# Kernel tuning notes

Measured on AMD Instinct MI355X. Metric: run time of the kernel, lower is better.

## Reference

```python
import jax, jax.numpy as jnp
import numpy as np

N_Q = 4  # QuantumSampler is hard-wired to 4 qubits (16-dim statevector)


def _build_tables():
    """Static permutation for the CNOT chain and Z-sign table, computed once in numpy."""
    n = N_Q
    dim = 1 << n
    cnots = [(i, (i + 1) % n) for i in range(n)]  # (0,1),(1,2),(2,3),(3,0)
    fmap = np.empty(dim, dtype=np.int64)
    for i in range(dim):
        bits = [(i >> (n - 1 - w)) & 1 for w in range(n)]  # wire w <-> bit (n-1-w)
        for c, t in cnots:
            if bits[c]:
                bits[t] ^= 1
        fmap[i] = sum(b << (n - 1 - w) for w, b in enumerate(bits))
    finv = np.argsort(fmap)  # new_state[j] = old_state[finv[j]]
    signs = np.array([[1.0 - 2.0 * ((j >> (n - 1 - w)) & 1) for w in range(n)]
                      for j in range(dim)], dtype=np.float32)  # <Z_w> signs per basis state
    return jnp.asarray(finv), jnp.asarray(signs)

PERM, SIGNS = _build_tables()


def quantum_gate_probs(q, theta):
    """Simulate: RX(q_w) then RX(theta_w) per wire (angles add), CNOT chain, <Z> per wire, softmax.
    q: [B,4] encoder angles; theta: [4] trainable angles. Returns [B,4] gate probabilities."""
    half = 0.5 * (q + theta)                      # RX(a)RX(b) = RX(a+b)
    c = jnp.cos(half).astype(jnp.complex64)       # amplitude on |0>
    s = (jnp.sin(half).astype(jnp.complex64)) * (-1j)  # amplitude on |1> is -i sin(a/2)
    a = jnp.stack([c, s], axis=-1)                # [B,4,2] single-qubit states
    a0, a1, a2, a3 = a[:, 0], a[:, 1], a[:, 2], a[:, 3]
    # product state |psi> = a0 (x) a1 (x) a2 (x) a3  -> [B,2,2,2,2] -> [B,16]
    st = (a0[:, :, None, None, None] * a1[:, None, :, None, None]
          * a2[:, None, None, :, None] * a3[:, None, None, None, :])
    st = st.reshape(q.shape[0], 16)[:, PERM]      # apply CNOT chain (amplitude permutation)
    probs = st.real ** 2 + st.imag ** 2           # [B,16]
    exps = probs @ SIGNS                          # [B,4] Pauli-Z expectations per wire
    return jax.nn.softmax(exps, axis=-1)


def setup_inputs() -> dict:
    key = jax.random.key(0)
    ks = jax.random.split(key, 8)
    T, B, D, H = 256, 128, 1024, 1024
    inputs = jax.random.normal(ks[0], (T, B, D), dtype=jnp.float32)
    sc_d = 1.0 / np.sqrt(D)
    sc_h = 1.0 / np.sqrt(H)
    return {
        "inputs": inputs,
        "Wi": jax.random.normal(ks[1], (H, D), dtype=jnp.float32) * sc_d,
        "bi": jnp.zeros((H,), dtype=jnp.float32),
        "Wh": jax.random.normal(ks[2], (H, H), dtype=jnp.float32) * sc_h,
        "bh": jnp.zeros((H,), dtype=jnp.float32),
        "Wq": jax.random.normal(ks[3], (4, H), dtype=jnp.float32) * sc_h,
        "bq": jnp.zeros((4,), dtype=jnp.float32),
        "theta": jax.random.uniform(ks[4], (4,), dtype=jnp.float32, minval=-np.pi, maxval=np.pi),
    }


def reference(inputs, Wi, bi, Wh, bh, Wq, bq, theta):
    T, B, _ = inputs.shape
    H = Wi.shape[0]
    hx0 = jnp.zeros((B, H), dtype=inputs.dtype)
    cx0 = jnp.zeros((B, H), dtype=inputs.dtype)

    def step(carry, x):
        hx, cx = carry
        combined = x @ Wi.T + bi + hx @ Wh.T + bh   # [B,H]
        qin = combined @ Wq.T + bq                  # [B,4]
        gates = quantum_gate_probs(qin, theta)      # [B,4]
        f, i_, g, o = gates[:, 0:1], gates[:, 1:2], gates[:, 2:3], gates[:, 3:4]
        cx = f * cx + i_ * jnp.tanh(g)              # broadcast [B,1]*[B,H]
        hx = o * jnp.tanh(cx)
        return (hx, cx), hx

    (hx, cx), ys = jax.lax.scan(step, (hx0, cx0), inputs)
    return ys, hx, cx
```

## Files before the change

### kernel.cpp

```cpp
#include <hip/hip_runtime.h>

#define T_STEPS 256
#define BATCH   128
#define DIM     1024
#define NROWS   (T_STEPS * BATCH)

typedef float vfloat4 __attribute__((ext_vector_type(4)));

#define WS_M     0
#define WS_VP    4096

__global__ __launch_bounds__(256) void k_prep(const float* __restrict__ Wi,
                                              const float* __restrict__ Wh,
                                              const float* __restrict__ bi,
                                              const float* __restrict__ bh,
                                              const float* __restrict__ Wq,
                                              float* __restrict__ M,
                                              float* __restrict__ vpart) {
    int blk  = blockIdx.x;
    int tid  = threadIdx.x;
    int wave = tid >> 6;
    int lane = tid & 63;

    if (blk < 16) {
        int d = blk * 64 + lane;
        const float* wq = Wq + wave * DIM;
        float acc = 0.f;
        for (int j = 0; j < DIM; j += 8) {
            #pragma unroll
            for (int u = 0; u < 8; u++)
                acc += wq[j + u] * Wi[(size_t)(j + u) * DIM + d];
        }
        M[wave * DIM + d] = acc;
    } else {
        int bb = blk - 16;
        __shared__ float red[4][8];
        int j0 = bb * 16 + wave * 4;
        float sv0 = 0.f, sv1 = 0.f, sv2 = 0.f, sv3 = 0.f;
        float sc0 = 0.f, sc1 = 0.f, sc2 = 0.f, sc3 = 0.f;
        #pragma unroll
        for (int jj = 0; jj < 4; jj++) {
            int j = j0 + jj;
            const float4* row = (const float4*)(Wh + (size_t)j * DIM);
            float s = 0.f;
            #pragma unroll
            for (int k = 0; k < 4; k++) {
                float4 t4 = row[k * 64 + lane];
                s += t4.x + t4.y + t4.z + t4.w;
            }
            #pragma unroll
            for (int off = 32; off; off >>= 1) s += __shfl_xor(s, off, 64);
            float bbias = bi[j] + bh[j];
            float q0 = Wq[0 * DIM + j], q1 = Wq[1 * DIM + j];
            float q2 = Wq[2 * DIM + j], q3 = Wq[3 * DIM + j];
            sv0 += q0 * s;  sc0 += q0 * bbias;
            sv1 += q1 * s;  sc1 += q1 * bbias;
            sv2 += q2 * s;  sc2 += q2 * bbias;
            sv3 += q3 * s;  sc3 += q3 * bbias;
        }
        if (lane == 0) {
            red[wave][0] = sv0; red[wave][1] = sv1; red[wave][2] = sv2; red[wave][3] = sv3;
            red[wave][4] = sc0; red[wave][5] = sc1; red[wave][6] = sc2; red[wave][7] = sc3;
        }
        __syncthreads();
        if (tid < 8)
            vpart[bb * 8 + tid] = red[0][tid] + red[1][tid] + red[2][tid] + red[3][tid];
    }
}

__device__ __forceinline__ float fast_tanh(float x) {
    float e = __expf(2.f * x);
    return (e - 1.f) * __builtin_amdgcn_rcpf(e + 1.f);
}

__device__ __forceinline__ void rec_step(float4 qv,
                                         float b0, float b1, float b2, float b3,
                                         float v0, float v1, float v2, float v3,
                                         float& h, float& c) {
    float z0 = __cosf(qv.x + b0 + h * v0);
    float z1 = __cosf(qv.y + b1 + h * v1);
    float z2 = __cosf(qv.z + b2 + h * v2);
    float z3 = __cosf(qv.w + b3 + h * v3);
    float e1 = z0 * z1;
    float e2 = e1 * z2;
    float e3 = e2 * z3;
    float e0 = z1 * z2 * z3;
    float x0 = __expf(e0), x1 = __expf(e1), x2 = __expf(e2), x3 = __expf(e3);
    float inv = __builtin_amdgcn_rcpf(x0 + x1 + x2 + x3);
    float f  = x0 * inv;
    float i_ = x1 * inv;
    float g  = x2 * inv;
    float o  = x3 * inv;
    c = f * c + i_ * fast_tanh(g);
    h = o * fast_tanh(c);
}

__global__ __launch_bounds__(512) void k_main(const float* __restrict__ x,
                                              const float* __restrict__ bq,
                                              const float* __restrict__ theta,
                                              const float* __restrict__ ws,
                                              float* __restrict__ out)
{
    __shared__ float4 qrow[T_STEPS];
    const float*  M   = ws + WS_M;
    const float4* vp4 = (const float4*)(ws + WS_VP);

    const int b    = blockIdx.x;
    const int tid  = threadIdx.x;
    const int wave = tid >> 6;
    const int lane = tid & 63;

    {
        float4 m[4][4];
        #pragma unroll
        for (int w = 0; w < 4; w++)
            #pragma unroll
            for (int k = 0; k < 4; k++)
                m[w][k] = *(const float4*)(M + w * DIM + k * 256 + lane * 4);

        for (int t = wave; t < T_STEPS; t += 8) {
            const float4* row = (const float4*)(x + ((size_t)t * BATCH + b) * DIM);
            float a0 = 0.f, a1 = 0.f, a2 = 0.f, a3 = 0.f;
            #pragma unroll
            for (int k = 0; k < 4; k++) {
                float4 xv = row[k * 64 + lane];
                a0 += xv.x * m[0][k].x + xv.y * m[0][k].y + xv.z * m[0][k].z + xv.w * m[0][k].w;
                a1 += xv.x * m[1][k].x + xv.y * m[1][k].y + xv.z * m[1][k].z + xv.w * m[1][k].w;
                a2 += xv.x * m[2][k].x + xv.y * m[2][k].y + xv.z * m[2][k].z + xv.w * m[2][k].w;
                a3 += xv.x * m[3][k].x + xv.y * m[3][k].y + xv.z * m[3][k].z + xv.w * m[3][k].w;
            }
            #pragma unroll
            for (int off = 32; off; off >>= 1) {
                a0 += __shfl_xor(a0, off, 64);
                a1 += __shfl_xor(a1, off, 64);
                a2 += __shfl_xor(a2, off, 64);
                a3 += __shfl_xor(a3, off, 64);
            }
            if (lane == 0) qrow[t] = make_float4(a0, a1, a2, a3);
        }
    }
    __syncthreads();
    if (wave >= 4) return;

    float4 sa = vp4[lane * 2];
    float4 sc = vp4[lane * 2 + 1];
    #pragma unroll
    for (int off = 32; off; off >>= 1) {
        sa.x += __shfl_xor(sa.x, off, 64);  sa.y += __shfl_xor(sa.y, off, 64);
        sa.z += __shfl_xor(sa.z, off, 64);  sa.w += __shfl_xor(sa.w, off, 64);
        sc.x += __shfl_xor(sc.x, off, 64);  sc.y += __shfl_xor(sc.y, off, 64);
        sc.z += __shfl_xor(sc.z, off, 64);  sc.w += __shfl_xor(sc.w, off, 64);
    }
    const float v0 = sa.x, v1 = sa.y, v2 = sa.z, v3 = sa.w;
    const float b0 = sc.x + bq[0] + theta[0];
    const float b1 = sc.y + bq[1] + theta[1];
    const float b2 = sc.z + bq[2] + theta[2];
    const float b3 = sc.w + bq[3] + theta[3];

    float h = 0.f, c = 0.f;

    #define EMIT_H(tt)                                                           \
        do {                                                                     \
            vfloat4 vv = {h, h, h, h};                                           \
            __builtin_nontemporal_store(vv,                                      \
                (vfloat4*)(out + ((size_t)(tt) * BATCH + b) * DIM + wave * 256)  \
                    + lane);                                                     \
        } while (0)

    float4 q0 = qrow[0], q1 = qrow[1], q2 = qrow[2], q3 = qrow[3];
    float4 q4 = qrow[4], q5 = qrow[5], q6 = qrow[6], q7 = qrow[7];

    for (int t = 0; t < T_STEPS; t += 8) {
        float4 n0, n1, n2, n3, n4, n5, n6, n7;
        if (t + 8 < T_STEPS) {
            n0 = qrow[t + 8];  n1 = qrow[t + 9];
            n2 = qrow[t + 10]; n3 = qrow[t + 11];
            n4 = qrow[t + 12]; n5 = qrow[t + 13];
            n6 = qrow[t + 14]; n7 = qrow[t + 15];
        }
        rec_step(q0, b0, b1, b2, b3, v0, v1, v2, v3, h, c); EMIT_H(t + 0);
        rec_step(q1, b0, b1, b2, b3, v0, v1, v2, v3, h, c); EMIT_H(t + 1);
        rec_step(q2, b0, b1, b2, b3, v0, v1, v2, v3, h, c); EMIT_H(t + 2);
        rec_step(q3, b0, b1, b2, b3, v0, v1, v2, v3, h, c); EMIT_H(t + 3);
        rec_step(q4, b0, b1, b2, b3, v0, v1, v2, v3, h, c); EMIT_H(t + 4);
        rec_step(q5, b0, b1, b2, b3, v0, v1, v2, v3, h, c); EMIT_H(t + 5);
        rec_step(q6, b0, b1, b2, b3, v0, v1, v2, v3, h, c); EMIT_H(t + 6);
        rec_step(q7, b0, b1, b2, b3, v0, v1, v2, v3, h, c); EMIT_H(t + 7);
        q0 = n0; q1 = n1; q2 = n2; q3 = n3; q4 = n4; q5 = n5; q6 = n6; q7 = n7;
    }
    #undef EMIT_H

    vfloat4 hv = {h, h, h, h};
    vfloat4 cv = {c, c, c, c};
    __builtin_nontemporal_store(hv,
        (vfloat4*)(out + ((size_t)NROWS + b) * DIM + wave * 256) + lane);
    __builtin_nontemporal_store(cv,
        (vfloat4*)(out + ((size_t)NROWS + BATCH + b) * DIM + wave * 256) + lane);
}

extern "C" void kernel_launch(void* const* d_in, const int* in_sizes, int n_in,
                              void* d_out, int out_size, void* d_ws, size_t ws_size,
                              hipStream_t stream) {
    const float* inputs = (const float*)d_in[0];
    const float* Wi     = (const float*)d_in[1];
    const float* bi     = (const float*)d_in[2];
    const float* Wh     = (const float*)d_in[3];
    const float* bh     = (const float*)d_in[4];
    const float* Wq     = (const float*)d_in[5];
    const float* bq     = (const float*)d_in[6];
    const float* theta  = (const float*)d_in[7];
    float* out = (float*)d_out;
    float* ws  = (float*)d_ws;

    float* M     = ws + WS_M;
    float* vpart = ws + WS_VP;

    k_prep<<<80,    256, 0, stream>>>(Wi, Wh, bi, bh, Wq, M, vpart);
    k_main<<<BATCH, 512, 0, stream>>>(inputs, bq, theta, ws, out);
}
```

Baseline: 305.2 us.

## Split each batch row across two blocks exchanging projections via global flag

Launches two blocks per batch element. Each block projects half of the timesteps, publishes its partial q-rows to global workspace, and spin-waits on a per-batch atomic counter before reading the other half. Both blocks then replay the full recurrence redundantly, and each stores only the outputs for its own timestep parity. The aim is to use more CUs for the memory-bound input projection and to split the output writes. The cost is an inter-block spin barrier that assumes both paired blocks are co-resident, which risks a stall or deadlock if they are not.

```diff
diff --git a/kernel.cpp b/kernel.cpp
--- a/kernel.cpp
+++ b/kernel.cpp
@@ -9,20 +9,27 @@
 
 #define WS_M     0
 #define WS_VP    4096
+#define WS_FLAG  4608
+#define WS_QX    8192
 
 __global__ __launch_bounds__(256) void k_prep(const float* __restrict__ Wi,
                                               const float* __restrict__ Wh,
                                               const float* __restrict__ bi,
                                               const float* __restrict__ bh,
                                               const float* __restrict__ Wq,
-                                              float* __restrict__ M,
-                                              float* __restrict__ vpart) {
+                                              float* __restrict__ ws) {
+    float*    M     = ws + WS_M;
+    float*    vpart = ws + WS_VP;
+    unsigned* flag  = (unsigned*)(ws + WS_FLAG);
+
     int blk  = blockIdx.x;
     int tid  = threadIdx.x;
     int wave = tid >> 6;
     int lane = tid & 63;
 
     if (blk < 16) {
+        if (blk == 0 && tid < BATCH) flag[tid] = 0u;
+
         int d = blk * 64 + lane;
         const float* wq = Wq + wave * DIM;
         float acc = 0.f;
@@ -98,14 +105,17 @@
 __global__ __launch_bounds__(512) void k_main(const float* __restrict__ x,
                                               const float* __restrict__ bq,
                                               const float* __restrict__ theta,
-                                              const float* __restrict__ ws,
+                                              float* __restrict__ ws,
                                               float* __restrict__ out)
 {
     __shared__ float4 qrow[T_STEPS];
-    const float*  M   = ws + WS_M;
-    const float4* vp4 = (const float4*)(ws + WS_VP);
-
-    const int b    = blockIdx.x;
+    const float*  M    = ws + WS_M;
+    const float4* vp4  = (const float4*)(ws + WS_VP);
+    unsigned*     flag = (unsigned*)(ws + WS_FLAG);
+    float*        qxg  = ws + WS_QX;
+
+    const int b    = blockIdx.x >> 1;
+    const int s    = blockIdx.x & 1;
     const int tid  = threadIdx.x;
     const int wave = tid >> 6;
     const int lane = tid & 63;
@@ -118,7 +128,9 @@
             for (int k = 0; k < 4; k++)
                 m[w][k] = *(const float4*)(M + w * DIM + k * 256 + lane * 4);
 
-        for (int t = wave; t < T_STEPS; t += 8) {
+        #pragma unroll 2
+        for (int j = 0; j < 16; ++j) {
+            int t = s + 2 * (wave + 8 * j);
             const float4* row = (const float4*)(x + ((size_t)t * BATCH + b) * DIM);
             float a0 = 0.f, a1 = 0.f, a2 = 0.f, a3 = 0.f;
             #pragma unroll
@@ -138,6 +150,39 @@
             }
             if (lane == 0) qrow[t] = make_float4(a0, a1, a2, a3);
         }
+    }
+    __syncthreads();
+
+    if (tid < 256) {
+        int t    = s + 2 * (tid >> 1);
+        int half = tid & 1;
+        float2 d = ((const float2*)qrow)[t * 2 + half];
+        unsigned long long u = ((unsigned long long)__float_as_uint(d.y) << 32)
+                             |  (unsigned long long)__float_as_uint(d.x);
+        __hip_atomic_store(
+            (unsigned long long*)(qxg + ((size_t)b * 256 + t) * 4 + half * 2),
+            u, __ATOMIC_RELAXED, __HIP_MEMORY_SCOPE_AGENT);
+    }
+    __syncthreads();
+    if (tid == 0) {
+        __hip_atomic_fetch_add(&flag[b], 1u, __ATOMIC_RELAXED, __HIP_MEMORY_SCOPE_AGENT);
+        for (int k = 0; k < (1 << 20); ++k) {
+            if (__hip_atomic_load(&flag[b], __ATOMIC_RELAXED, __HIP_MEMORY_SCOPE_AGENT) >= 2u)
+                break;
+            __builtin_amdgcn_s_sleep(2);
+        }
+    }
+    __syncthreads();
+
+    if (tid < 256) {
+        int t    = (s ^ 1) + 2 * (tid >> 1);
+        int half = tid & 1;
+        unsigned long long u = __hip_atomic_load(
+            (const unsigned long long*)(qxg + ((size_t)b * 256 + t) * 4 + half * 2),
+            __ATOMIC_RELAXED, __HIP_MEMORY_SCOPE_AGENT);
+        ((float2*)qrow)[t * 2 + half] =
+            make_float2(__uint_as_float((unsigned)u),
+                        __uint_as_float((unsigned)(u >> 32)));
     }
     __syncthreads();
     if (wave >= 4) return;
@@ -161,10 +206,12 @@
 
     #define EMIT_H(tt)                                                           \
         do {                                                                     \
-            vfloat4 vv = {h, h, h, h};                                           \
-            __builtin_nontemporal_store(vv,                                      \
-                (vfloat4*)(out + ((size_t)(tt) * BATCH + b) * DIM + wave * 256)  \
-                    + lane);                                                     \
+            if ((((tt) & 1)) == s) {                                             \
+                vfloat4 vv = {h, h, h, h};                                       \
+                __builtin_nontemporal_store(vv,                                  \
+                    (vfloat4*)(out + ((size_t)(tt) * BATCH + b) * DIM            \
+                               + wave * 256) + lane);                            \
+            }                                                                    \
         } while (0)
 
     float4 q0 = qrow[0], q1 = qrow[1], q2 = qrow[2], q3 = qrow[3];
@@ -190,12 +237,15 @@
     }
     #undef EMIT_H
 
-    vfloat4 hv = {h, h, h, h};
-    vfloat4 cv = {c, c, c, c};
-    __builtin_nontemporal_store(hv,
-        (vfloat4*)(out + ((size_t)NROWS + b) * DIM + wave * 256) + lane);
-    __builtin_nontemporal_store(cv,
-        (vfloat4*)(out + ((size_t)NROWS + BATCH + b) * DIM + wave * 256) + lane);
+    if (s == 0) {
+        vfloat4 hv = {h, h, h, h};
+        __builtin_nontemporal_store(hv,
+            (vfloat4*)(out + ((size_t)NROWS + b) * DIM + wave * 256) + lane);
+    } else {
+        vfloat4 cv = {c, c, c, c};
+        __builtin_nontemporal_store(cv,
+            (vfloat4*)(out + ((size_t)NROWS + BATCH + b) * DIM + wave * 256) + lane);
+    }
 }
 
 extern "C" void kernel_launch(void* const* d_in, const int* in_sizes, int n_in,
@@ -212,9 +262,6 @@
     float* out = (float*)d_out;
     float* ws  = (float*)d_ws;
 
-    float* M     = ws + WS_M;
-    float* vpart = ws + WS_VP;
-
-    k_prep<<<80,    256, 0, stream>>>(Wi, Wh, bi, bh, Wq, M, vpart);
-    k_main<<<BATCH, 512, 0, stream>>>(inputs, bq, theta, ws, out);
-}
+    k_prep<<<80,  256, 0, stream>>>(Wi, Wh, bi, bh, Wq, ws);
+    k_main<<<256, 512, 0, stream>>>(inputs, bq, theta, ws, out);
+}
```

New measurement: 307.3 us. Within noise of the previous version (+0.7%).
